# Optimization experiments

Measured on AMD Instinct MI355X. Metric: run time of the kernel, lower is better.

The kernel has to match this reference:

```python
import jax, jax.numpy as jnp
import numpy as np

NEG_INF = -1e9  # large negative for masking (avoid NaN rows under -inf with fully masked rows)
LEAKY_SLOPE = 0.2

def setup_inputs() -> dict:
    key = jax.random.key(0)
    k1, k2, k3, k4, k5 = jax.random.split(key, 5)
    N, in_dim, out_dim = 8192, 512, 64
    x = jax.random.normal(k1, (N, in_dim), dtype=jnp.float32)
    adj = jax.random.randint(k2, (N, N), 0, 2, dtype=jnp.int32)
    W = jax.random.normal(k3, (out_dim, in_dim), dtype=jnp.float32) * (1.0 / np.sqrt(in_dim))
    a_src = jax.random.normal(k4, (out_dim,), dtype=jnp.float32)
    a_dst = jax.random.normal(k5, (out_dim,), dtype=jnp.float32)
    return {"x": x, "adj": adj, "W": W, "a_src": a_src, "a_dst": a_dst}

def reference(x, adj, W, a_src, a_dst):
    # Linear projection: Wh[n, d]
    Wh = x @ W.T
    # Additive GAT attention: e[i, j] = LeakyReLU(a_src . Wh_i + a_dst . Wh_j)
    s = Wh @ a_src  # [N]
    d = Wh @ a_dst  # [N]
    e = jax.nn.leaky_relu(s[:, None] + d[None, :], negative_slope=LEAKY_SLOPE)  # [N, N]
    e = jnp.where(adj > 0, e, NEG_INF)
    alpha = jax.nn.softmax(e, axis=1)  # [N, N]
    # Dropout on alpha is identity in eval/reference mode.
    h_prime = alpha @ Wh  # [N, out_dim]
    return h_prime
```

## Files before the change

kernel.cpp:

```cpp
#include <hip/hip_runtime.h>
#include <hip/hip_bf16.h>

#define GN 8192
#define IN_DIM 512
#define ODIM 64
#define SLOPE 0.2f
#define NT2 2
#define JSPLIT2 8

typedef __attribute__((ext_vector_type(4))) float  f32x4;
typedef __attribute__((ext_vector_type(4))) int    i32x4;
typedef __attribute__((ext_vector_type(8))) short  bf16x8;
typedef __attribute__((ext_vector_type(4))) unsigned short u16x4;

static __device__ __forceinline__ float bf2f(unsigned short u) {
    return __uint_as_float(((unsigned)u) << 16);
}
static __device__ __forceinline__ unsigned short f2bf(float f) {
    union { float f; unsigned u; } c; c.f = f;
    unsigned b = c.u;
    return (unsigned short)((b + 0x7fffu + ((b >> 16) & 1u)) >> 16);
}

static __device__ __forceinline__ bf16x8 load8(const void* p, size_t off, int f32) {
    if (f32) {
        f32x4 lo = *(const f32x4*)((const float*)p + off);
        f32x4 hi = *(const f32x4*)((const float*)p + off + 4);
        bf16x8 r;
        #pragma unroll
        for (int q = 0; q < 4; ++q) {
            r[q]     = (short)f2bf(lo[q]);
            r[4 + q] = (short)f2bf(hi[q]);
        }
        return r;
    }
    return *(const bf16x8*)((const ushort*)p + off);
}

extern "C" __global__ __launch_bounds__(256)
void gat_pack(const int* __restrict__ adj, unsigned* __restrict__ gbm)
{
    const size_t ui = (size_t)blockIdx.x * 256 + threadIdx.x;
    const int* p = adj + ui * 32;
    unsigned w = 0;
    #pragma unroll
    for (int c = 0; c < 8; ++c) {
        i32x4 v = ((const i32x4*)p)[c];
        #pragma unroll
        for (int q = 0; q < 4; ++q)
            w |= (v[q] > 0 ? 1u : 0u) << (c * 4 + q);
    }
    gbm[ui] = w;
}

extern "C" __global__ __launch_bounds__(256)
void gat_proj(const void* __restrict__ x_, const void* __restrict__ W_,
              const void* __restrict__ as_, const void* __restrict__ ad_,
              ushort* __restrict__ WhTp, float* __restrict__ s_arr,
              float* __restrict__ E1, float* __restrict__ E2,
              int* __restrict__ dmax_bits, int* __restrict__ dflag,
              float* __restrict__ accum, float* __restrict__ lsum)
{
    {
        f32x4 z = {0.f, 0.f, 0.f, 0.f};
        f32x4* ap = (f32x4*)(accum + (size_t)blockIdx.x * 4096);
        #pragma unroll
        for (int k = 0; k < 4; ++k) ap[k * 256 + threadIdx.x] = z;
        if (threadIdx.x < 64) lsum[blockIdx.x * 64 + threadIdx.x] = 0.f;
    }
    const int wave = threadIdx.x >> 6;
    const int lane = threadIdx.x & 63;
    unsigned xw = ((const unsigned*)x_)[lane];
    unsigned ef = (xw >> 23) & 0xffu;
    unsigned long long vt = __ballot(ef > 60u && ef < 180u);
    const int f32 = (__popcll(vt) >= 32) ? 1 : 0;
    if (blockIdx.x == 0 && threadIdx.x == 0) *dflag = f32;

    const int quad = lane >> 4;
    const int lq   = lane & 15;
    const int i0   = blockIdx.x * 64 + wave * 16;

    f32x4 acc[4] = {{0,0,0,0},{0,0,0,0},{0,0,0,0},{0,0,0,0}};
    const size_t arow = (size_t)(i0 + lq) * IN_DIM;
    #pragma unroll 2
    for (int k0 = 0; k0 < IN_DIM; k0 += 32) {
        const int kk = k0 + quad * 8;
        bf16x8 a  = load8(x_, arow + kk, f32);
        bf16x8 b0 = load8(W_, (size_t)( 0 + lq) * IN_DIM + kk, f32);
        bf16x8 b1 = load8(W_, (size_t)(16 + lq) * IN_DIM + kk, f32);
        bf16x8 b2 = load8(W_, (size_t)(32 + lq) * IN_DIM + kk, f32);
        bf16x8 b3 = load8(W_, (size_t)(48 + lq) * IN_DIM + kk, f32);
        acc[0] = __builtin_amdgcn_mfma_f32_16x16x32_bf16(a, b0, acc[0], 0, 0, 0);
        acc[1] = __builtin_amdgcn_mfma_f32_16x16x32_bf16(a, b1, acc[1], 0, 0, 0);
        acc[2] = __builtin_amdgcn_mfma_f32_16x16x32_bf16(a, b2, acc[2], 0, 0, 0);
        acc[3] = __builtin_amdgcn_mfma_f32_16x16x32_bf16(a, b3, acc[3], 0, 0, 0);
    }
    float av_s[4], av_d[4];
    #pragma unroll
    for (int t = 0; t < 4; ++t) {
        const int n = t * 16 + lq;
        av_s[t] = f32 ? ((const float*)as_)[n] : bf2f(((const ushort*)as_)[n]);
        av_d[t] = f32 ? ((const float*)ad_)[n] : bf2f(((const ushort*)ad_)[n]);
    }
    #pragma unroll
    for (int t = 0; t < 4; ++t) {
        u16x4 pk;
        #pragma unroll
        for (int r = 0; r < 4; ++r) pk[r] = f2bf(acc[t][r]);
        const size_t hw = ((size_t)((i0 >> 3) + (quad >> 1)) * 64 + t * 16 + lq) * 8
                          + (quad & 1) * 4;
        *(u16x4*)(WhTp + hw) = pk;
    }
    float ps[4], pd[4];
    #pragma unroll
    for (int r = 0; r < 4; ++r) {
        float s = 0.f, d = 0.f;
        #pragma unroll
        for (int t = 0; t < 4; ++t) {
            s = fmaf(acc[t][r], av_s[t], s);
            d = fmaf(acc[t][r], av_d[t], d);
        }
        #pragma unroll
        for (int off = 1; off < 16; off <<= 1) {
            s += __shfl_xor(s, off);
            d += __shfl_xor(d, off);
        }
        ps[r] = s; pd[r] = d;
    }
    if (lq == 0) {
        float dmx = -1e30f;
        #pragma unroll
        for (int r = 0; r < 4; ++r) {
            const int n = i0 + quad * 4 + r;
            const float dv = pd[r];
            s_arr[n] = ps[r];
            E1[n] = __expf(fminf(dv, 87.f));
            E2[n] = __expf(SLOPE * dv);
            dmx = fmaxf(dmx, dv);
        }
        if (dmx > 0.f) atomicMax(dmax_bits, __float_as_int(dmx));
    }
}

extern "C" __global__ __launch_bounds__(256)
void gat_attn(const unsigned char* __restrict__ gbm,
              const ushort* __restrict__ WhTp,
              const float* __restrict__ s_arr,
              const float* __restrict__ E1, const float* __restrict__ E2,
              const int* __restrict__ dmax_bits,
              float* __restrict__ accum, float* __restrict__ lsum)
{
    __shared__ float lE[2 * NT2 * 512];
    const int b    = blockIdx.x;
    const int ib   = b & 127;
    const int js0  = b >> 7;
    const int wave = threadIdx.x >> 6;
    const int lane = threadIdx.x & 63;
    const int quad = lane >> 4;
    const int lq   = lane & 15;
    const int i0   = ib * 64;
    const int i    = i0 + wave * 16 + lq;

    {
        const int m0 = threadIdx.x * 4;
        const int gcol = (js0 * NT2 + (m0 >> 9)) * 512 + (m0 & 511);
        *(f32x4*)&lE[m0]        = *(const f32x4*)(E1 + gcol);
        *(f32x4*)&lE[1024 + m0] = *(const f32x4*)(E2 + gcol);
    }

    const float dmax = __int_as_float(*dmax_bits);
    const float si  = s_arr[i];
    const float tbv = si + dmax;
    const float mi  = fmaxf(tbv, SLOPE * tbv);
    const float Aw  = __expf(si - mi);
    const float Bw  = __expf(SLOPE * si - mi);

    const unsigned char* mrow = gbm + (size_t)i * (GN / 8);
    const int colbase = js0 * NT2 * 512;

    f32x4 acc0 = {0,0,0,0}, acc1 = {0,0,0,0}, acc2 = {0,0,0,0}, acc3 = {0,0,0,0};
    f32x4 acc4 = {0,0,0,0};
    bf16x8 ones;
    #pragma unroll
    for (int q = 0; q < 8; ++q) ones[q] = (short)0x3F80;

    unsigned bm = *(const unsigned*)(mrow + (colbase >> 3));
    bf16x8 b0, b1, b2, b3;
    {
        const int col = colbase;
        const ushort* nb = WhTp + ((size_t)(col >> 3) + quad) * 512;
        b0 = *(const bf16x8*)(nb + ( 0 + lq) * 8);
        b1 = *(const bf16x8*)(nb + (16 + lq) * 8);
        b2 = *(const bf16x8*)(nb + (32 + lq) * 8);
        b3 = *(const bf16x8*)(nb + (48 + lq) * 8);
    }
    __syncthreads();

    #pragma unroll 1
    for (int t = 0; t < NT2; ++t) {
        #pragma unroll
        for (int it = 0; it < 16; ++it) {
            const int u = t * 16 + it;
            const int un   = (u < NT2 * 16 - 1) ? u + 1 : u;
            const int ncol = colbase + un * 32;
            const unsigned nbm = *(const unsigned*)(mrow + (ncol >> 3));
            const ushort* nb = WhTp + ((size_t)(ncol >> 3) + quad) * 512;
            const bf16x8 nb0 = *(const bf16x8*)(nb + ( 0 + lq) * 8);
            const bf16x8 nb1 = *(const bf16x8*)(nb + (16 + lq) * 8);
            const bf16x8 nb2 = *(const bf16x8*)(nb + (32 + lq) * 8);
            const bf16x8 nb3 = *(const bf16x8*)(nb + (48 + lq) * 8);
            const float* pe = lE + u * 32 + quad * 8;
            const f32x4 e1a = *(const f32x4*)pe;
            const f32x4 e1b = *(const f32x4*)(pe + 4);
            const f32x4 e2a = *(const f32x4*)(pe + 1024);
            const f32x4 e2b = *(const f32x4*)(pe + 1028);
            const unsigned m8 = (bm >> (quad * 8)) & 0xffu;
            float w[8];
            #pragma unroll
            for (int q = 0; q < 4; ++q) {
                const float w0 = fmaxf(Aw * e1a[q], Bw * e2a[q]);
                const float w1 = fmaxf(Aw * e1b[q], Bw * e2b[q]);
                w[q]     = ((m8 >> q) & 1u) ? w0 : 0.f;
                w[4 + q] = ((m8 >> (4 + q)) & 1u) ? w1 : 0.f;
            }
            union { bf16x8 v; __hip_bfloat162 h[4]; } af;
            #pragma unroll
            for (int q = 0; q < 4; ++q)
                af.h[q] = __float22bfloat162_rn(make_float2(w[2 * q], w[2 * q + 1]));
            acc0 = __builtin_amdgcn_mfma_f32_16x16x32_bf16(af.v, b0, acc0, 0, 0, 0);
            acc1 = __builtin_amdgcn_mfma_f32_16x16x32_bf16(af.v, b1, acc1, 0, 0, 0);
            acc2 = __builtin_amdgcn_mfma_f32_16x16x32_bf16(af.v, b2, acc2, 0, 0, 0);
            acc3 = __builtin_amdgcn_mfma_f32_16x16x32_bf16(af.v, b3, acc3, 0, 0, 0);
            acc4 = __builtin_amdgcn_mfma_f32_16x16x32_bf16(af.v, ones, acc4, 0, 0, 0);
            bm = nbm; b0 = nb0; b1 = nb1; b2 = nb2; b3 = nb3;
        }
    }

    const int orow = i0 + wave * 16 + quad * 4;
    if (lq == 0) {
        #pragma unroll
        for (int r = 0; r < 4; ++r) atomicAdd(&lsum[orow + r], acc4[r]);
    }
    #pragma unroll
    for (int r = 0; r < 4; ++r) {
        atomicAdd(&accum[(size_t)(orow + r) * ODIM +  0 + lq], acc0[r]);
        atomicAdd(&accum[(size_t)(orow + r) * ODIM + 16 + lq], acc1[r]);
        atomicAdd(&accum[(size_t)(orow + r) * ODIM + 32 + lq], acc2[r]);
        atomicAdd(&accum[(size_t)(orow + r) * ODIM + 48 + lq], acc3[r]);
    }
}

extern "C" __global__ __launch_bounds__(256)
void gat_final(const float* __restrict__ accum, const float* __restrict__ lsum,
               const int* __restrict__ flag, void* __restrict__ out)
{
    const int idx = blockIdx.x * 256 + threadIdx.x;
    const float v = accum[idx] / lsum[idx >> 6];
    if (*flag) ((float*)out)[idx] = v;
    else       ((ushort*)out)[idx] = f2bf(v);
}

extern "C" void kernel_launch(void* const* d_in, const int* in_sizes, int n_in,
                              void* d_out, int out_size, void* d_ws, size_t ws_size,
                              hipStream_t stream)
{
    const void* x     = d_in[0];
    const int*  adj   = (const int*)d_in[1];
    const void* W     = d_in[2];
    const void* a_src = d_in[3];
    const void* a_dst = d_in[4];

    char* ws = (char*)d_ws;
    size_t off = 0;
    int* dmax_bits = (int*)(ws + off);  off += 128;
    int* dflag = (int*)(ws + off);      off += 128;
    size_t zero_bytes = off;
    float* accum = (float*)(ws + off);  off += (size_t)GN * ODIM * 4;
    float* lsum  = (float*)(ws + off);  off += (size_t)GN * 4;
    float* s_arr = (float*)(ws + off);  off += (size_t)GN * 4;
    float* E1    = (float*)(ws + off);  off += (size_t)GN * 4;
    float* E2    = (float*)(ws + off);  off += (size_t)GN * 4;
    ushort* WhTp = (ushort*)(ws + off); off += (size_t)ODIM * GN * 2;
    unsigned* gbm = (unsigned*)(ws + off); off += (size_t)GN * (GN / 8);

    hipMemsetAsync(ws, 0, zero_bytes, stream);
    gat_pack<<<GN * (GN / 32) / 256, 256, 0, stream>>>(adj, gbm);
    gat_proj<<<GN / 64, 256, 0, stream>>>(x, W, a_src, a_dst,
                                          WhTp, s_arr, E1, E2, dmax_bits, dflag,
                                          accum, lsum);
    gat_attn<<<128 * JSPLIT2, 256, 0, stream>>>((const unsigned char*)gbm, WhTp,
                                                s_arr, E1, E2, dmax_bits,
                                                accum, lsum);
    gat_final<<<GN * ODIM / 256, 256, 0, stream>>>(accum, lsum, dflag, d_out);
}
```

Baseline: 460.9 us.

## Replace atomic split-K accumulation with per-split partial slabs reduced in final kernel

```diff
diff --git a/kernel.cpp b/kernel.cpp
--- a/kernel.cpp
+++ b/kernel.cpp
@@ -5,8 +5,9 @@
 #define IN_DIM 512
 #define ODIM 64
 #define SLOPE 0.2f
-#define NT2 2
-#define JSPLIT2 8
+#define KSPL 4
+#define KCOLS (GN / KSPL)
+#define KITER (KCOLS / 32)
 
 typedef __attribute__((ext_vector_type(4))) float  f32x4;
 typedef __attribute__((ext_vector_type(4))) int    i32x4;
@@ -58,16 +59,8 @@
               const void* __restrict__ as_, const void* __restrict__ ad_,
               ushort* __restrict__ WhTp, float* __restrict__ s_arr,
               float* __restrict__ E1, float* __restrict__ E2,
-              int* __restrict__ dmax_bits, int* __restrict__ dflag,
-              float* __restrict__ accum, float* __restrict__ lsum)
-{
-    {
-        f32x4 z = {0.f, 0.f, 0.f, 0.f};
-        f32x4* ap = (f32x4*)(accum + (size_t)blockIdx.x * 4096);
-        #pragma unroll
-        for (int k = 0; k < 4; ++k) ap[k * 256 + threadIdx.x] = z;
-        if (threadIdx.x < 64) lsum[blockIdx.x * 64 + threadIdx.x] = 0.f;
-    }
+              int* __restrict__ dmax_bits, int* __restrict__ dflag)
+{
     const int wave = threadIdx.x >> 6;
     const int lane = threadIdx.x & 63;
     unsigned xw = ((const unsigned*)x_)[lane];
@@ -142,15 +135,15 @@
     }
 }
 
-extern "C" __global__ __launch_bounds__(256)
+extern "C" __global__ __launch_bounds__(256, 2)
 void gat_attn(const unsigned char* __restrict__ gbm,
               const ushort* __restrict__ WhTp,
               const float* __restrict__ s_arr,
               const float* __restrict__ E1, const float* __restrict__ E2,
               const int* __restrict__ dmax_bits,
-              float* __restrict__ accum, float* __restrict__ lsum)
-{
-    __shared__ float lE[2 * NT2 * 512];
+              float* __restrict__ part, float* __restrict__ prs)
+{
+    __shared__ float lE[2 * KCOLS];
     const int b    = blockIdx.x;
     const int ib   = b & 127;
     const int js0  = b >> 7;
@@ -160,12 +153,14 @@
     const int lq   = lane & 15;
     const int i0   = ib * 64;
     const int i    = i0 + wave * 16 + lq;
+    const int colbase = js0 * KCOLS;
 
     {
-        const int m0 = threadIdx.x * 4;
-        const int gcol = (js0 * NT2 + (m0 >> 9)) * 512 + (m0 & 511);
-        *(f32x4*)&lE[m0]        = *(const f32x4*)(E1 + gcol);
-        *(f32x4*)&lE[1024 + m0] = *(const f32x4*)(E2 + gcol);
+        const int m0 = threadIdx.x * 8;
+        *(f32x4*)&lE[m0]              = *(const f32x4*)(E1 + colbase + m0);
+        *(f32x4*)&lE[m0 + 4]          = *(const f32x4*)(E1 + colbase + m0 + 4);
+        *(f32x4*)&lE[KCOLS + m0]      = *(const f32x4*)(E2 + colbase + m0);
+        *(f32x4*)&lE[KCOLS + m0 + 4]  = *(const f32x4*)(E2 + colbase + m0 + 4);
     }
 
     const float dmax = __int_as_float(*dmax_bits);
@@ -176,7 +171,6 @@
     const float Bw  = __expf(SLOPE * si - mi);
 
     const unsigned char* mrow = gbm + (size_t)i * (GN / 8);
-    const int colbase = js0 * NT2 * 512;
 
     f32x4 acc0 = {0,0,0,0}, acc1 = {0,0,0,0}, acc2 = {0,0,0,0}, acc3 = {0,0,0,0};
     f32x4 acc4 = {0,0,0,0};
@@ -187,8 +181,7 @@
     unsigned bm = *(const unsigned*)(mrow + (colbase >> 3));
     bf16x8 b0, b1, b2, b3;
     {
-        const int col = colbase;
-        const ushort* nb = WhTp + ((size_t)(col >> 3) + quad) * 512;
+        const ushort* nb = WhTp + ((size_t)(colbase >> 3) + quad) * 512;
         b0 = *(const bf16x8*)(nb + ( 0 + lq) * 8);
         b1 = *(const bf16x8*)(nb + (16 + lq) * 8);
         b2 = *(const bf16x8*)(nb + (32 + lq) * 8);
@@ -196,66 +189,70 @@
     }
     __syncthreads();
 
-    #pragma unroll 1
-    for (int t = 0; t < NT2; ++t) {
-        #pragma unroll
-        for (int it = 0; it < 16; ++it) {
-            const int u = t * 16 + it;
-            const int un   = (u < NT2 * 16 - 1) ? u + 1 : u;
-            const int ncol = colbase + un * 32;
-            const unsigned nbm = *(const unsigned*)(mrow + (ncol >> 3));
-            const ushort* nb = WhTp + ((size_t)(ncol >> 3) + quad) * 512;
-            const bf16x8 nb0 = *(const bf16x8*)(nb + ( 0 + lq) * 8);
-            const bf16x8 nb1 = *(const bf16x8*)(nb + (16 + lq) * 8);
-            const bf16x8 nb2 = *(const bf16x8*)(nb + (32 + lq) * 8);
-            const bf16x8 nb3 = *(const bf16x8*)(nb + (48 + lq) * 8);
-            const float* pe = lE + u * 32 + quad * 8;
-            const f32x4 e1a = *(const f32x4*)pe;
-            const f32x4 e1b = *(const f32x4*)(pe + 4);
-            const f32x4 e2a = *(const f32x4*)(pe + 1024);
-            const f32x4 e2b = *(const f32x4*)(pe + 1028);
-            const unsigned m8 = (bm >> (quad * 8)) & 0xffu;
-            float w[8];
-            #pragma unroll
-            for (int q = 0; q < 4; ++q) {
-                const float w0 = fmaxf(Aw * e1a[q], Bw * e2a[q]);
-                const float w1 = fmaxf(Aw * e1b[q], Bw * e2b[q]);
-                w[q]     = ((m8 >> q) & 1u) ? w0 : 0.f;
-                w[4 + q] = ((m8 >> (4 + q)) & 1u) ? w1 : 0.f;
-            }
-            union { bf16x8 v; __hip_bfloat162 h[4]; } af;
-            #pragma unroll
-            for (int q = 0; q < 4; ++q)
-                af.h[q] = __float22bfloat162_rn(make_float2(w[2 * q], w[2 * q + 1]));
-            acc0 = __builtin_amdgcn_mfma_f32_16x16x32_bf16(af.v, b0, acc0, 0, 0, 0);
-            acc1 = __builtin_amdgcn_mfma_f32_16x16x32_bf16(af.v, b1, acc1, 0, 0, 0);
-            acc2 = __builtin_amdgcn_mfma_f32_16x16x32_bf16(af.v, b2, acc2, 0, 0, 0);
-            acc3 = __builtin_amdgcn_mfma_f32_16x16x32_bf16(af.v, b3, acc3, 0, 0, 0);
-            acc4 = __builtin_amdgcn_mfma_f32_16x16x32_bf16(af.v, ones, acc4, 0, 0, 0);
-            bm = nbm; b0 = nb0; b1 = nb1; b2 = nb2; b3 = nb3;
-        }
+    #pragma unroll 4
+    for (int u = 0; u < KITER; ++u) {
+        const int un   = (u < KITER - 1) ? u + 1 : u;
+        const int ncol = colbase + un * 32;
+        const unsigned nbm = *(const unsigned*)(mrow + (ncol >> 3));
+        const ushort* nb = WhTp + ((size_t)(ncol >> 3) + quad) * 512;
+        const bf16x8 nb0 = *(const bf16x8*)(nb + ( 0 + lq) * 8);
+        const bf16x8 nb1 = *(const bf16x8*)(nb + (16 + lq) * 8);
+        const bf16x8 nb2 = *(const bf16x8*)(nb + (32 + lq) * 8);
+        const bf16x8 nb3 = *(const bf16x8*)(nb + (48 + lq) * 8);
+        const float* pe = lE + u * 32 + quad * 8;
+        const f32x4 e1a = *(const f32x4*)pe;
+        const f32x4 e1b = *(const f32x4*)(pe + 4);
+        const f32x4 e2a = *(const f32x4*)(pe + KCOLS);
+        const f32x4 e2b = *(const f32x4*)(pe + KCOLS + 4);
+        const unsigned m8 = (bm >> (quad * 8)) & 0xffu;
+        float w[8];
+        #pragma unroll
+        for (int q = 0; q < 4; ++q) {
+            const float w0 = fmaxf(Aw * e1a[q], Bw * e2a[q]);
+            const float w1 = fmaxf(Aw * e1b[q], Bw * e2b[q]);
+            w[q]     = ((m8 >> q) & 1u) ? w0 : 0.f;
+            w[4 + q] = ((m8 >> (4 + q)) & 1u) ? w1 : 0.f;
+        }
+        union { bf16x8 v; __hip_bfloat162 h[4]; } af;
+        #pragma unroll
+        for (int q = 0; q < 4; ++q)
+            af.h[q] = __float22bfloat162_rn(make_float2(w[2 * q], w[2 * q + 1]));
+        acc0 = __builtin_amdgcn_mfma_f32_16x16x32_bf16(af.v, b0, acc0, 0, 0, 0);
+        acc1 = __builtin_amdgcn_mfma_f32_16x16x32_bf16(af.v, b1, acc1, 0, 0, 0);
+        acc2 = __builtin_amdgcn_mfma_f32_16x16x32_bf16(af.v, b2, acc2, 0, 0, 0);
+        acc3 = __builtin_amdgcn_mfma_f32_16x16x32_bf16(af.v, b3, acc3, 0, 0, 0);
+        acc4 = __builtin_amdgcn_mfma_f32_16x16x32_bf16(af.v, ones, acc4, 0, 0, 0);
+        bm = nbm; b0 = nb0; b1 = nb1; b2 = nb2; b3 = nb3;
     }
 
     const int orow = i0 + wave * 16 + quad * 4;
+    float* pslab = part + ((size_t)js0 * GN + orow) * ODIM;
     if (lq == 0) {
         #pragma unroll
-        for (int r = 0; r < 4; ++r) atomicAdd(&lsum[orow + r], acc4[r]);
+        for (int r = 0; r < 4; ++r) prs[js0 * GN + orow + r] = acc4[r];
     }
     #pragma unroll
     for (int r = 0; r < 4; ++r) {
-        atomicAdd(&accum[(size_t)(orow + r) * ODIM +  0 + lq], acc0[r]);
-        atomicAdd(&accum[(size_t)(orow + r) * ODIM + 16 + lq], acc1[r]);
-        atomicAdd(&accum[(size_t)(orow + r) * ODIM + 32 + lq], acc2[r]);
-        atomicAdd(&accum[(size_t)(orow + r) * ODIM + 48 + lq], acc3[r]);
+        pslab[r * ODIM +  0 + lq] = acc0[r];
+        pslab[r * ODIM + 16 + lq] = acc1[r];
+        pslab[r * ODIM + 32 + lq] = acc2[r];
+        pslab[r * ODIM + 48 + lq] = acc3[r];
     }
 }
 
 extern "C" __global__ __launch_bounds__(256)
-void gat_final(const float* __restrict__ accum, const float* __restrict__ lsum,
+void gat_final(const float* __restrict__ part, const float* __restrict__ prs,
                const int* __restrict__ flag, void* __restrict__ out)
 {
     const int idx = blockIdx.x * 256 + threadIdx.x;
-    const float v = accum[idx] / lsum[idx >> 6];
+    const int row = idx >> 6;
+    float a = 0.f, s = 0.f;
+    #pragma unroll
+    for (int k = 0; k < KSPL; ++k) {
+        a += part[(size_t)k * GN * ODIM + idx];
+        s += prs[k * GN + row];
+    }
+    const float v = a / s;
     if (*flag) ((float*)out)[idx] = v;
     else       ((ushort*)out)[idx] = f2bf(v);
 }
@@ -275,21 +272,20 @@
     int* dmax_bits = (int*)(ws + off);  off += 128;
     int* dflag = (int*)(ws + off);      off += 128;
     size_t zero_bytes = off;
-    float* accum = (float*)(ws + off);  off += (size_t)GN * ODIM * 4;
-    float* lsum  = (float*)(ws + off);  off += (size_t)GN * 4;
     float* s_arr = (float*)(ws + off);  off += (size_t)GN * 4;
     float* E1    = (float*)(ws + off);  off += (size_t)GN * 4;
     float* E2    = (float*)(ws + off);  off += (size_t)GN * 4;
     ushort* WhTp = (ushort*)(ws + off); off += (size_t)ODIM * GN * 2;
     unsigned* gbm = (unsigned*)(ws + off); off += (size_t)GN * (GN / 8);
+    float* part  = (float*)(ws + off);  off += (size_t)KSPL * GN * ODIM * 4;
+    float* prs   = (float*)(ws + off);  off += (size_t)KSPL * GN * 4;
 
     hipMemsetAsync(ws, 0, zero_bytes, stream);
     gat_pack<<<GN * (GN / 32) / 256, 256, 0, stream>>>(adj, gbm);
     gat_proj<<<GN / 64, 256, 0, stream>>>(x, W, a_src, a_dst,
-                                          WhTp, s_arr, E1, E2, dmax_bits, dflag,
-                                          accum, lsum);
-    gat_attn<<<128 * JSPLIT2, 256, 0, stream>>>((const unsigned char*)gbm, WhTp,
-                                                s_arr, E1, E2, dmax_bits,
-                                                accum, lsum);
-    gat_final<<<GN * ODIM / 256, 256, 0, stream>>>(accum, lsum, dflag, d_out);
-}
+                                          WhTp, s_arr, E1, E2, dmax_bits, dflag);
+    gat_attn<<<128 * KSPL, 256, 0, stream>>>((const unsigned char*)gbm, WhTp,
+                                             s_arr, E1, E2, dmax_bits,
+                                             part, prs);
+    gat_final<<<GN * ODIM / 256, 256, 0, stream>>>(part, prs, dflag, d_out);
+}
```

After: 455.2 us. About the same (-1.2%).
